# Performance work log

Hardware: AMD Instinct MI355X
Metric: run time of the kernel (lower is better)

Reference implementation:

```python
import jax, jax.numpy as jnp
import numpy as np

DIM = 768
HEADS = 8
HIDDEN = 3072
B, Hs, Ws = 16, 32, 32
N = Hs * Ws
LN_EPS = 1e-5


def setup_inputs() -> dict:
    key = jax.random.key(0)
    ks = jax.random.split(key, 10)
    s = lambda *sh: 0.02
    return {
        "x": jax.random.normal(ks[0], (B, N, DIM), jnp.float32),
        "Wq": jax.random.normal(ks[1], (DIM, DIM), jnp.float32) * 0.02,
        "temperature": jnp.ones((HEADS, 1, 1), jnp.float32),
        "fc1_w": jax.random.normal(ks[2], (HIDDEN, DIM), jnp.float32) * 0.02,
        "fc1_b": jnp.zeros((HIDDEN,), jnp.float32),
        "dw_w": jax.random.normal(ks[3], (HIDDEN, 1, 3, 3), jnp.float32) * 0.1,
        "dw_b": jnp.zeros((HIDDEN,), jnp.float32),
        "gamma": jnp.ones((HIDDEN,), jnp.float32),
        "fc2_w": jax.random.normal(ks[4], (DIM, HIDDEN), jnp.float32) * 0.02,
        "fc2_b": jnp.zeros((DIM,), jnp.float32),
        "ln_w": jnp.ones((DIM,), jnp.float32),
        "ln_b": jnp.zeros((DIM,), jnp.float32),
        "H": Hs,
        "W": Ws,
    }


def _dwconv(x, w, b, H, W):
    # x: (B, N, hidden) -> depthwise 3x3, pad 1 -> (B, N, hidden)
    Bn, Nn, Ch = x.shape
    img = x.transpose(0, 2, 1).reshape(Bn, Ch, H, W)
    out = jax.lax.conv_general_dilated(
        img, w, window_strides=(1, 1), padding=((1, 1), (1, 1)),
        dimension_numbers=("NCHW", "OIHW", "NCHW"), feature_group_count=Ch)
    out = out + b[None, :, None, None]
    return out.reshape(Bn, Ch, Nn).transpose(0, 2, 1)


def _layernorm(x, w, b):
    mu = x.mean(-1, keepdims=True)
    var = ((x - mu) ** 2).mean(-1, keepdims=True)
    return (x - mu) * jax.lax.rsqrt(var + LN_EPS) * w + b


def reference(x, Wq, temperature, fc1_w, fc1_b, dw_w, dw_b, gamma,
              fc2_w, fc2_b, ln_w, ln_b, H, W):
    # gpd_ratio == active_ratio == 1 -> pre/post scalings cancel
    Bn, Nn, C = x.shape
    h = temperature.shape[0]
    Ch = C // h
    # q/k/v heads: (B, h, N, Ch)
    q = (x @ Wq.T).reshape(Bn, Nn, h, Ch).transpose(0, 2, 1, 3)
    kv = x.reshape(Bn, Nn, h, Ch).transpose(0, 2, 1, 3)
    # channel attention: softmax over N, pool k over Ch, sigmoid gate
    qs = jax.nn.softmax(q, axis=-2).transpose(0, 1, 3, 2)      # (B,h,Ch,N)
    kp = jax.nn.softmax(kv, axis=-2).mean(-1, keepdims=True)    # (B,h,N,1)
    attn = jax.nn.sigmoid(qs @ kp) * temperature                # (B,h,Ch,1)
    # MLP on v (== x after scaling cancels): fc1 -> dwconv residual -> fc2 -> LN
    h1 = x @ fc1_w.T + fc1_b                                    # (B,N,hidden)
    h2 = gamma * _dwconv(h1, dw_w, dw_b, H, W) + h1
    v = _layernorm(h2 @ fc2_w.T + fc2_b, ln_w, ln_b)            # (B,N,C)
    v = v.reshape(Bn, Nn, h, Ch).transpose(0, 2, 1, 3)          # (B,h,N,Ch)
    prod = attn * v.transpose(0, 1, 3, 2)                       # (B,h,Ch,N)
    out = prod.transpose(0, 3, 1, 2).reshape(Bn, Nn, C)
    return out, prod.transpose(0, 1, 3, 2)
```

## Files before the change

### kernel.cpp

```cpp
#include <hip/hip_runtime.h>

#define BATCH 16
#define SEQ   1024
#define DIM   768
#define NHEAD 8
#define CHD   96
#define HID   3072
#define MTOT  (BATCH * SEQ)

using u16 = unsigned short;
typedef __attribute__((ext_vector_type(8))) short bf16x8;
typedef __attribute__((ext_vector_type(4))) float f32x4;

#define AS1 __attribute__((address_space(1)))
#define AS3 __attribute__((address_space(3)))

__device__ inline float bf2f(u16 u) {
    union { unsigned int i; float f; } v; v.i = ((unsigned int)u) << 16; return v.f;
}
__device__ inline u16 f2bf(float f) {
    union { float f; unsigned int i; } v; v.f = f;
    unsigned int r = v.i + 0x7FFFu + ((v.i >> 16) & 1u);
    return (u16)(r >> 16);
}

__device__ inline void gld16(const void* g, void* l) {
    __builtin_amdgcn_global_load_lds((AS1 const void*)g, (AS3 void*)l, 16, 0, 0);
}

__device__ inline void storeC(float* p, float v) { *p = v; }
__device__ inline void storeC(u16* p, float v) { *p = f2bf(v); }

template <bool HAS_BIAS, typename TC>
__global__ __launch_bounds__(256) void gemm_mfma(const u16* __restrict__ A,
                                                 const u16* __restrict__ B,
                                                 const float* __restrict__ bias,
                                                 TC* __restrict__ C,
                                                 int M, int N, int K) {
    __shared__ u16 As[128 * 32];
    __shared__ u16 Bs[128 * 32];
    const int tid = threadIdx.x;
    const int lane = tid & 63;
    const int m0 = blockIdx.y << 7, n0 = blockIdx.x << 7;
    const int wave = tid >> 6;
    const int wm = (wave >> 1) << 6, wn = (wave & 1) << 6;

    f32x4 acc[4][4] = {};

    const int row0 = tid >> 2;
    const int kc8 = (tid & 3) << 3;
    const u16* pa0 = A + (size_t)(m0 + row0) * K + kc8;
    const u16* pa1 = A + (size_t)(m0 + 64 + row0) * K + kc8;
    const u16* pb0 = B + (size_t)(n0 + row0) * K + kc8;
    const u16* pb1 = B + (size_t)(n0 + 64 + row0) * K + kc8;
    u16* da0 = &As[tid * 8];
    u16* da1 = &As[(256 + tid) * 8];
    u16* db0 = &Bs[tid * 8];
    u16* db1 = &Bs[(256 + tid) * 8];

    const int lrow = lane & 15;
    const int kgrp = (lane >> 4) << 3;

    for (int k0 = 0; k0 < K; k0 += 32) {
        gld16(pa0 + k0, da0);
        gld16(pa1 + k0, da1);
        gld16(pb0 + k0, db0);
        gld16(pb1 + k0, db1);
        __syncthreads();

        bf16x8 af[4], bfr[4];
#pragma unroll
        for (int i = 0; i < 4; ++i)
            af[i] = *(const bf16x8*)&As[(wm + i * 16 + lrow) * 32 + kgrp];
#pragma unroll
        for (int j = 0; j < 4; ++j)
            bfr[j] = *(const bf16x8*)&Bs[(wn + j * 16 + lrow) * 32 + kgrp];
#pragma unroll
        for (int i = 0; i < 4; ++i)
#pragma unroll
            for (int j = 0; j < 4; ++j)
                acc[i][j] = __builtin_amdgcn_mfma_f32_16x16x32_bf16(af[i], bfr[j], acc[i][j], 0, 0, 0);
        __syncthreads();
    }

    const int crow = (lane >> 4) << 2;
    const int ccol = lane & 15;
#pragma unroll
    for (int i = 0; i < 4; ++i) {
        const int gm = m0 + wm + i * 16 + crow;
#pragma unroll
        for (int j = 0; j < 4; ++j) {
            const int gn = n0 + wn + j * 16 + ccol;
            const float bv = HAS_BIAS ? bias[gn] : 0.f;
#pragma unroll
            for (int r = 0; r < 4; ++r)
                storeC(C + (size_t)(gm + r) * N + gn, acc[i][j][r] + bv);
        }
    }
}

__global__ __launch_bounds__(256) void cvt_f2bf(const float* __restrict__ in,
                                                u16* __restrict__ out, int n4) {
    int i = blockIdx.x * 256 + threadIdx.x;
    if (i >= n4) return;
    float4 v = reinterpret_cast<const float4*>(in)[i];
    ushort4 o;
    o.x = f2bf(v.x); o.y = f2bf(v.y); o.z = f2bf(v.z); o.w = f2bf(v.w);
    reinterpret_cast<ushort4*>(out)[i] = o;
}

template <typename T>
__global__ __launch_bounds__(256) void colsm_stats(const T* __restrict__ X,
                                                   float* __restrict__ Mo,
                                                   float* __restrict__ So,
                                                   int ncols) {
    const int tid = threadIdx.x, lane = tid & 63, chunk = tid >> 6;
    const int b = blockIdx.y;
    const int j = blockIdx.x * 64 + lane;
    const T* p = X + (size_t)b * SEQ * ncols + j;
    float m = -3.0e38f, s = 0.f;
    const int nEnd = (chunk + 1) << 8;
    for (int n = chunk << 8; n < nEnd; ++n) {
        float raw;
        if constexpr (sizeof(T) == 2) raw = bf2f(p[(size_t)n * ncols]);
        else raw = p[(size_t)n * ncols];
        float nm = fmaxf(m, raw);
        s = s * __expf(m - nm) + __expf(raw - nm);
        m = nm;
    }
    __shared__ float ms[4][64], ss[4][64];
    ms[chunk][lane] = m; ss[chunk][lane] = s;
    __syncthreads();
    if (tid < 64) {
        float M = fmaxf(fmaxf(ms[0][lane], ms[1][lane]), fmaxf(ms[2][lane], ms[3][lane]));
        float S = ss[0][lane] * __expf(ms[0][lane] - M) + ss[1][lane] * __expf(ms[1][lane] - M) +
                  ss[2][lane] * __expf(ms[2][lane] - M) + ss[3][lane] * __expf(ms[3][lane] - M);
        Mo[b * ncols + j] = M;
        So[b * ncols + j] = S;
    }
}

__global__ __launch_bounds__(256) void kp_k(const float* __restrict__ x,
                                            const float* __restrict__ Mx,
                                            const float* __restrict__ Sx,
                                            float* __restrict__ kp) {
    const int n = blockIdx.x, b = blockIdx.y, tid = threadIdx.x;
    __shared__ float p[DIM];
    const float* row = x + ((size_t)b * SEQ + n) * DIM;
#pragma unroll
    for (int q = 0; q < 3; ++q) {
        int j = tid + (q << 8);
        p[j] = __expf(row[j] - Mx[b * DIM + j]) / Sx[b * DIM + j];
    }
    __syncthreads();
    if (tid < NHEAD) {
        float s = 0.f;
        for (int c = 0; c < CHD; ++c) s += p[tid * CHD + c];
        kp[((size_t)b * NHEAD + tid) * SEQ + n] = s * (1.f / (float)CHD);
    }
}

__global__ __launch_bounds__(256) void attn_k(const u16* __restrict__ Q,
                                              const float* __restrict__ Mq,
                                              const float* __restrict__ Sq,
                                              const float* __restrict__ kp,
                                              const float* __restrict__ temp,
                                              float* __restrict__ attnv) {
    const int tid = threadIdx.x, lane = tid & 63, chunk = tid >> 6;
    const int b = blockIdx.y;
    const int j = blockIdx.x * 64 + lane;
    const int h = j / CHD;
    const float mq = Mq[b * DIM + j];
    const u16* qp = Q + (size_t)b * SEQ * DIM + j;
    const float* kpp = kp + ((size_t)b * NHEAD + h) * SEQ;
    float acc = 0.f;
    const int nEnd = (chunk + 1) << 8;
    for (int n = chunk << 8; n < nEnd; ++n)
        acc += __expf(bf2f(qp[(size_t)n * DIM]) - mq) * kpp[n];
    __shared__ float accs[4][64];
    accs[chunk][lane] = acc;
    __syncthreads();
    if (tid < 64) {
        float a = accs[0][lane] + accs[1][lane] + accs[2][lane] + accs[3][lane];
        float z = a / Sq[b * DIM + j];
        attnv[b * DIM + j] = temp[h] / (1.f + __expf(-z));
    }
}

__global__ __launch_bounds__(128) void dwconv_v(const u16* __restrict__ h1,
                                                const float* __restrict__ w,
                                                const float* __restrict__ dwb,
                                                const float* __restrict__ gamma,
                                                u16* __restrict__ h2) {
    const int g = blockIdx.x * 128 + threadIdx.x;
    const int y = blockIdx.y >> 2;
    const int xw0 = (blockIdx.y & 3) << 3;
    const int b = blockIdx.z;
    const int ch0 = g << 3;

    float wreg[8][9], bias2[8];
#pragma unroll
    for (int c = 0; c < 8; ++c) {
        const float gm = gamma[ch0 + c];
#pragma unroll
        for (int k = 0; k < 9; ++k) wreg[c][k] = gm * w[(ch0 + c) * 9 + k];
        wreg[c][4] += 1.0f;
        bias2[c] = gm * dwb[ch0 + c];
    }

    float acc[8][8];
#pragma unroll
    for (int xo = 0; xo < 8; ++xo)
#pragma unroll
        for (int c = 0; c < 8; ++c) acc[xo][c] = bias2[c];

    const u16* base = h1 + (size_t)b * SEQ * HID + ch0;
#pragma unroll
    for (int dy = 0; dy < 3; ++dy) {
        const int yy = y + dy - 1;
        if ((unsigned)yy > 31u) continue;
#pragma unroll
        for (int cr = -1; cr <= 8; ++cr) {
            const int col = xw0 + cr;
            if ((unsigned)col > 31u) continue;
            const uint4 v = *reinterpret_cast<const uint4*>(
                base + (size_t)((yy << 5) + col) * HID);
            float f[8];
            f[0] = bf2f((u16)(v.x & 0xffff)); f[1] = bf2f((u16)(v.x >> 16));
            f[2] = bf2f((u16)(v.y & 0xffff)); f[3] = bf2f((u16)(v.y >> 16));
            f[4] = bf2f((u16)(v.z & 0xffff)); f[5] = bf2f((u16)(v.w & 0xffff) * 0 + (u16)(v.z >> 16));
            f[6] = bf2f((u16)(v.w & 0xffff)); f[7] = bf2f((u16)(v.w >> 16));
            const int xlo = cr > 0 ? cr - 1 : 0;
            const int xhi = cr < 7 ? cr + 1 : 7;
#pragma unroll
            for (int xo = 0; xo < 8; ++xo) {
                if (xo < xlo || xo > xhi) continue;
                const int dx = cr - xo + 1;
#pragma unroll
                for (int c = 0; c < 8; ++c)
                    acc[xo][c] += f[c] * wreg[c][dy * 3 + dx];
            }
        }
    }

#pragma unroll
    for (int xo = 0; xo < 8; ++xo) {
        const int n = (y << 5) + xw0 + xo;
        uint4 o;
        o.x = (unsigned)f2bf(acc[xo][0]) | ((unsigned)f2bf(acc[xo][1]) << 16);
        o.y = (unsigned)f2bf(acc[xo][2]) | ((unsigned)f2bf(acc[xo][3]) << 16);
        o.z = (unsigned)f2bf(acc[xo][4]) | ((unsigned)f2bf(acc[xo][5]) << 16);
        o.w = (unsigned)f2bf(acc[xo][6]) | ((unsigned)f2bf(acc[xo][7]) << 16);
        *reinterpret_cast<uint4*>(h2 + ((size_t)b * SEQ + n) * HID + ch0) = o;
    }
}

__global__ __launch_bounds__(256) void ln_out_k(const u16* __restrict__ vpre,
                                                const float* __restrict__ lnw,
                                                const float* __restrict__ lnb,
                                                const float* __restrict__ attnv,
                                                float* __restrict__ out,
                                                float* __restrict__ out2) {
    const int n = blockIdx.x, b = blockIdx.y, tid = threadIdx.x;
    __shared__ float red[4];
    const u16* row = vpre + ((size_t)b * SEQ + n) * DIM;
    float v[3];
    float s = 0.f;
#pragma unroll
    for (int q = 0; q < 3; ++q) { v[q] = bf2f(row[tid + (q << 8)]); s += v[q]; }
#pragma unroll
    for (int o = 32; o; o >>= 1) s += __shfl_down(s, o, 64);
    if ((tid & 63) == 0) red[tid >> 6] = s;
    __syncthreads();
    const float mu = (red[0] + red[1] + red[2] + red[3]) * (1.f / (float)DIM);
    __syncthreads();
    float vs = 0.f;
#pragma unroll
    for (int q = 0; q < 3; ++q) { float d = v[q] - mu; vs += d * d; }
#pragma unroll
    for (int o = 32; o; o >>= 1) vs += __shfl_down(vs, o, 64);
    if ((tid & 63) == 0) red[tid >> 6] = vs;
    __syncthreads();
    const float rstd = rsqrtf((red[0] + red[1] + red[2] + red[3]) * (1.f / (float)DIM) + 1e-5f);
    const float* at = attnv + b * DIM;
    float* orow = out + ((size_t)b * SEQ + n) * DIM;
#pragma unroll
    for (int q = 0; q < 3; ++q) {
        int j = tid + (q << 8);
        float o = (v[q] - mu) * rstd * lnw[j] + lnb[j];
        o *= at[j];
        orow[j] = o;
        int h = j / CHD, c = j - h * CHD;
        out2[(((size_t)b * NHEAD + h) * SEQ + n) * CHD + c] = o;
    }
}

extern "C" void kernel_launch(void* const* d_in, const int* in_sizes, int n_in,
                              void* d_out, int out_size, void* d_ws, size_t ws_size,
                              hipStream_t stream) {
    const float* x     = (const float*)d_in[0];
    const float* Wq    = (const float*)d_in[1];
    const float* temp  = (const float*)d_in[2];
    const float* fc1w  = (const float*)d_in[3];
    const float* fc1b  = (const float*)d_in[4];
    const float* dww   = (const float*)d_in[5];
    const float* dwb   = (const float*)d_in[6];
    const float* gamma = (const float*)d_in[7];
    const float* fc2w  = (const float*)d_in[8];
    const float* fc2b  = (const float*)d_in[9];
    const float* lnw   = (const float*)d_in[10];
    const float* lnb   = (const float*)d_in[11];

    float* out  = (float*)d_out;
    float* out2 = out + (size_t)BATCH * SEQ * DIM;

    char* ws = (char*)d_ws;
    u16* xb     = (u16*)ws;
    u16* h1     = (u16*)(ws + 25165824);
    u16* Wqb    = (u16*)(ws + 125829120);
    u16* fc1wb  = (u16*)(ws + 127008768);
    u16* fc2wb  = (u16*)(ws + 131727360);
    float* Mx   = (float*)(ws + 136445952);
    float* Sx   = Mx + BATCH * DIM;
    float* Mq   = Sx + BATCH * DIM;
    float* Sq   = Mq + BATCH * DIM;
    float* kp   = Sq + BATCH * DIM;
    float* attnv = kp + BATCH * NHEAD * SEQ;
    u16* vpreb  = xb;

    u16* Qb = (u16*)d_out;
    u16* h2 = (u16*)d_out;

    cvt_f2bf<<<(MTOT * DIM / 4 + 255) / 256, 256, 0, stream>>>(x, xb, MTOT * DIM / 4);
    cvt_f2bf<<<(DIM * DIM / 4 + 255) / 256, 256, 0, stream>>>(Wq, Wqb, DIM * DIM / 4);
    cvt_f2bf<<<(HID * DIM / 4 + 255) / 256, 256, 0, stream>>>(fc1w, fc1wb, HID * DIM / 4);
    cvt_f2bf<<<(DIM * HID / 4 + 255) / 256, 256, 0, stream>>>(fc2w, fc2wb, DIM * HID / 4);

    gemm_mfma<false, u16><<<dim3(DIM / 128, MTOT / 128), 256, 0, stream>>>(
        xb, Wqb, nullptr, Qb, MTOT, DIM, DIM);
    colsm_stats<float><<<dim3(DIM / 64, BATCH), 256, 0, stream>>>(x, Mx, Sx, DIM);
    colsm_stats<u16><<<dim3(DIM / 64, BATCH), 256, 0, stream>>>(Qb, Mq, Sq, DIM);
    kp_k<<<dim3(SEQ, BATCH), 256, 0, stream>>>(x, Mx, Sx, kp);
    attn_k<<<dim3(DIM / 64, BATCH), 256, 0, stream>>>(Qb, Mq, Sq, kp, temp, attnv);

    gemm_mfma<true, u16><<<dim3(HID / 128, MTOT / 128), 256, 0, stream>>>(
        xb, fc1wb, fc1b, h1, MTOT, HID, DIM);
    dwconv_v<<<dim3(3, 128, BATCH), 128, 0, stream>>>(h1, dww, dwb, gamma, h2);
    gemm_mfma<true, u16><<<dim3(DIM / 128, MTOT / 128), 256, 0, stream>>>(
        h2, fc2wb, fc2b, vpreb, MTOT, DIM, HID);
    ln_out_k<<<dim3(SEQ, BATCH), 256, 0, stream>>>(vpreb, lnw, lnb, attnv, out, out2);
}
```

Baseline: 464.4 us.

## Rework GEMM with K=64 swizzled LDS tiles and XCD remap, fuse small kernels

```diff
diff --git a/kernel.cpp b/kernel.cpp
--- a/kernel.cpp
+++ b/kernel.cpp
@@ -28,63 +28,71 @@
     __builtin_amdgcn_global_load_lds((AS1 const void*)g, (AS3 void*)l, 16, 0, 0);
 }
 
-__device__ inline void storeC(float* p, float v) { *p = v; }
-__device__ inline void storeC(u16* p, float v) { *p = f2bf(v); }
-
-template <bool HAS_BIAS, typename TC>
-__global__ __launch_bounds__(256) void gemm_mfma(const u16* __restrict__ A,
-                                                 const u16* __restrict__ B,
-                                                 const float* __restrict__ bias,
-                                                 TC* __restrict__ C,
-                                                 int M, int N, int K) {
-    __shared__ u16 As[128 * 32];
-    __shared__ u16 Bs[128 * 32];
+template <bool HAS_BIAS>
+__global__ __launch_bounds__(256) void gemm128(const u16* __restrict__ A,
+                                               const u16* __restrict__ B,
+                                               const float* __restrict__ bias,
+                                               u16* __restrict__ C,
+                                               int M, int N, int K) {
+    __shared__ u16 As[128 * 64];
+    __shared__ u16 Bs[128 * 64];
     const int tid = threadIdx.x;
     const int lane = tid & 63;
-    const int m0 = blockIdx.y << 7, n0 = blockIdx.x << 7;
     const int wave = tid >> 6;
     const int wm = (wave >> 1) << 6, wn = (wave & 1) << 6;
 
+    const int nwg = gridDim.x;
+    const int wg = blockIdx.x;
+    const int lid = (wg & 7) * (nwg >> 3) + (wg >> 3);
+    const int nbx = N >> 7;
+    const int mb = lid / nbx, nb = lid - mb * nbx;
+    const int m0 = mb << 7, n0 = nb << 7;
+
+    const int srow = tid >> 3;
+    const int sce = ((tid & 7) << 3) ^ ((srow & 7) << 3);
+    const u16* pa = A + (size_t)(m0 + srow) * K + sce;
+    const u16* pb = B + (size_t)(n0 + srow) * K + sce;
+    const size_t rstep = (size_t)32 * K;
+
+    const int lrow = lane & 15;
+    const int ksl8 = (lane >> 4) << 3;
+    const int swz = (lrow & 7) << 3;
+    const int c0 = ksl8 ^ swz;
+    const int c1 = (32 + ksl8) ^ swz;
+
     f32x4 acc[4][4] = {};
 
-    const int row0 = tid >> 2;
-    const int kc8 = (tid & 3) << 3;
-    const u16* pa0 = A + (size_t)(m0 + row0) * K + kc8;
-    const u16* pa1 = A + (size_t)(m0 + 64 + row0) * K + kc8;
-    const u16* pb0 = B + (size_t)(n0 + row0) * K + kc8;
-    const u16* pb1 = B + (size_t)(n0 + 64 + row0) * K + kc8;
-    u16* da0 = &As[tid * 8];
-    u16* da1 = &As[(256 + tid) * 8];
-    u16* db0 = &Bs[tid * 8];
-    u16* db1 = &Bs[(256 + tid) * 8];
-
-    const int lrow = lane & 15;
-    const int kgrp = (lane >> 4) << 3;
-
-    for (int k0 = 0; k0 < K; k0 += 32) {
-        gld16(pa0 + k0, da0);
-        gld16(pa1 + k0, da1);
-        gld16(pb0 + k0, db0);
-        gld16(pb1 + k0, db1);
+    for (int k0 = 0; k0 < K; k0 += 64) {
+#pragma unroll
+        for (int q = 0; q < 4; ++q) {
+            gld16(pa + k0 + q * rstep, &As[q * 2048 + tid * 8]);
+            gld16(pb + k0 + q * rstep, &Bs[q * 2048 + tid * 8]);
+        }
         __syncthreads();
 
-        bf16x8 af[4], bfr[4];
+        bf16x8 af[4], bf[4];
+#pragma unroll
+        for (int i = 0; i < 4; ++i) af[i] = *(const bf16x8*)&As[(wm + i * 16 + lrow) * 64 + c0];
+#pragma unroll
+        for (int j = 0; j < 4; ++j) bf[j] = *(const bf16x8*)&Bs[(wn + j * 16 + lrow) * 64 + c0];
 #pragma unroll
         for (int i = 0; i < 4; ++i)
-            af[i] = *(const bf16x8*)&As[(wm + i * 16 + lrow) * 32 + kgrp];
-#pragma unroll
-        for (int j = 0; j < 4; ++j)
-            bfr[j] = *(const bf16x8*)&Bs[(wn + j * 16 + lrow) * 32 + kgrp];
+#pragma unroll
+            for (int j = 0; j < 4; ++j)
+                acc[i][j] = __builtin_amdgcn_mfma_f32_16x16x32_bf16(af[i], bf[j], acc[i][j], 0, 0, 0);
+#pragma unroll
+        for (int i = 0; i < 4; ++i) af[i] = *(const bf16x8*)&As[(wm + i * 16 + lrow) * 64 + c1];
+#pragma unroll
+        for (int j = 0; j < 4; ++j) bf[j] = *(const bf16x8*)&Bs[(wn + j * 16 + lrow) * 64 + c1];
 #pragma unroll
         for (int i = 0; i < 4; ++i)
 #pragma unroll
             for (int j = 0; j < 4; ++j)
-                acc[i][j] = __builtin_amdgcn_mfma_f32_16x16x32_bf16(af[i], bfr[j], acc[i][j], 0, 0, 0);
+                acc[i][j] = __builtin_amdgcn_mfma_f32_16x16x32_bf16(af[i], bf[j], acc[i][j], 0, 0, 0);
         __syncthreads();
     }
 
-    const int crow = (lane >> 4) << 2;
-    const int ccol = lane & 15;
+    const int crow = (lane >> 4) << 2, ccol = lane & 15;
 #pragma unroll
     for (int i = 0; i < 4; ++i) {
         const int gm = m0 + wm + i * 16 + crow;
@@ -94,36 +102,47 @@
             const float bv = HAS_BIAS ? bias[gn] : 0.f;
 #pragma unroll
             for (int r = 0; r < 4; ++r)
-                storeC(C + (size_t)(gm + r) * N + gn, acc[i][j][r] + bv);
+                C[(size_t)(gm + r) * N + gn] = f2bf(acc[i][j][r] + bv);
         }
     }
 }
 
-__global__ __launch_bounds__(256) void cvt_f2bf(const float* __restrict__ in,
-                                                u16* __restrict__ out, int n4) {
+__global__ __launch_bounds__(256) void cvt_all(const float* __restrict__ x,
+                                               const float* __restrict__ Wq,
+                                               const float* __restrict__ w1,
+                                               const float* __restrict__ w2,
+                                               u16* __restrict__ xb,
+                                               u16* __restrict__ Wqb,
+                                               u16* __restrict__ w1b,
+                                               u16* __restrict__ w2b) {
+    const int E0 = MTOT * DIM / 4;
+    const int E1 = E0 + DIM * DIM / 4;
+    const int E2 = E1 + HID * DIM / 4;
+    const int E3 = E2 + DIM * HID / 4;
     int i = blockIdx.x * 256 + threadIdx.x;
-    if (i >= n4) return;
-    float4 v = reinterpret_cast<const float4*>(in)[i];
+    if (i >= E3) return;
+    const float* in; u16* out; int k;
+    if (i < E0)      { in = x;  out = xb;  k = i; }
+    else if (i < E1) { in = Wq; out = Wqb; k = i - E0; }
+    else if (i < E2) { in = w1; out = w1b; k = i - E1; }
+    else             { in = w2; out = w2b; k = i - E2; }
+    float4 v = reinterpret_cast<const float4*>(in)[k];
     ushort4 o;
     o.x = f2bf(v.x); o.y = f2bf(v.y); o.z = f2bf(v.z); o.w = f2bf(v.w);
-    reinterpret_cast<ushort4*>(out)[i] = o;
-}
-
-template <typename T>
-__global__ __launch_bounds__(256) void colsm_stats(const T* __restrict__ X,
+    reinterpret_cast<ushort4*>(out)[k] = o;
+}
+
+__global__ __launch_bounds__(256) void colsm_stats(const u16* __restrict__ X,
                                                    float* __restrict__ Mo,
-                                                   float* __restrict__ So,
-                                                   int ncols) {
+                                                   float* __restrict__ So) {
     const int tid = threadIdx.x, lane = tid & 63, chunk = tid >> 6;
     const int b = blockIdx.y;
     const int j = blockIdx.x * 64 + lane;
-    const T* p = X + (size_t)b * SEQ * ncols + j;
+    const u16* p = X + (size_t)b * SEQ * DIM + j;
     float m = -3.0e38f, s = 0.f;
     const int nEnd = (chunk + 1) << 8;
     for (int n = chunk << 8; n < nEnd; ++n) {
-        float raw;
-        if constexpr (sizeof(T) == 2) raw = bf2f(p[(size_t)n * ncols]);
-        else raw = p[(size_t)n * ncols];
+        float raw = bf2f(p[(size_t)n * DIM]);
         float nm = fmaxf(m, raw);
         s = s * __expf(m - nm) + __expf(raw - nm);
         m = nm;
@@ -135,22 +154,22 @@
         float M = fmaxf(fmaxf(ms[0][lane], ms[1][lane]), fmaxf(ms[2][lane], ms[3][lane]));
         float S = ss[0][lane] * __expf(ms[0][lane] - M) + ss[1][lane] * __expf(ms[1][lane] - M) +
                   ss[2][lane] * __expf(ms[2][lane] - M) + ss[3][lane] * __expf(ms[3][lane] - M);
-        Mo[b * ncols + j] = M;
-        So[b * ncols + j] = S;
-    }
-}
-
-__global__ __launch_bounds__(256) void kp_k(const float* __restrict__ x,
+        Mo[b * DIM + j] = M;
+        So[b * DIM + j] = S;
+    }
+}
+
+__global__ __launch_bounds__(256) void kp_k(const u16* __restrict__ x,
                                             const float* __restrict__ Mx,
                                             const float* __restrict__ Sx,
                                             float* __restrict__ kp) {
     const int n = blockIdx.x, b = blockIdx.y, tid = threadIdx.x;
     __shared__ float p[DIM];
-    const float* row = x + ((size_t)b * SEQ + n) * DIM;
+    const u16* row = x + ((size_t)b * SEQ + n) * DIM;
 #pragma unroll
     for (int q = 0; q < 3; ++q) {
         int j = tid + (q << 8);
-        p[j] = __expf(row[j] - Mx[b * DIM + j]) / Sx[b * DIM + j];
+        p[j] = __expf(bf2f(row[j]) - Mx[b * DIM + j]) / Sx[b * DIM + j];
     }
     __syncthreads();
     if (tid < NHEAD) {
@@ -160,29 +179,39 @@
     }
 }
 
-__global__ __launch_bounds__(256) void attn_k(const u16* __restrict__ Q,
-                                              const float* __restrict__ Mq,
-                                              const float* __restrict__ Sq,
-                                              const float* __restrict__ kp,
-                                              const float* __restrict__ temp,
-                                              float* __restrict__ attnv) {
+__global__ __launch_bounds__(256) void qattn_k(const u16* __restrict__ Q,
+                                               const float* __restrict__ kp,
+                                               const float* __restrict__ temp,
+                                               float* __restrict__ attnv) {
     const int tid = threadIdx.x, lane = tid & 63, chunk = tid >> 6;
     const int b = blockIdx.y;
     const int j = blockIdx.x * 64 + lane;
     const int h = j / CHD;
-    const float mq = Mq[b * DIM + j];
     const u16* qp = Q + (size_t)b * SEQ * DIM + j;
     const float* kpp = kp + ((size_t)b * NHEAD + h) * SEQ;
-    float acc = 0.f;
+    float m = -3.0e38f, s = 0.f, a = 0.f;
     const int nEnd = (chunk + 1) << 8;
-    for (int n = chunk << 8; n < nEnd; ++n)
-        acc += __expf(bf2f(qp[(size_t)n * DIM]) - mq) * kpp[n];
-    __shared__ float accs[4][64];
-    accs[chunk][lane] = acc;
+    for (int n = chunk << 8; n < nEnd; ++n) {
+        float q = bf2f(qp[(size_t)n * DIM]);
+        float nm = fmaxf(m, q);
+        float sc = __expf(m - nm), e = __expf(q - nm);
+        s = s * sc + e;
+        a = a * sc + e * kpp[n];
+        m = nm;
+    }
+    __shared__ float ms[4][64], ss[4][64], as_[4][64];
+    ms[chunk][lane] = m; ss[chunk][lane] = s; as_[chunk][lane] = a;
     __syncthreads();
     if (tid < 64) {
-        float a = accs[0][lane] + accs[1][lane] + accs[2][lane] + accs[3][lane];
-        float z = a / Sq[b * DIM + j];
+        float M = fmaxf(fmaxf(ms[0][lane], ms[1][lane]), fmaxf(ms[2][lane], ms[3][lane]));
+        float S = 0.f, A = 0.f;
+#pragma unroll
+        for (int c = 0; c < 4; ++c) {
+            float sc = __expf(ms[c][lane] - M);
+            S += ss[c][lane] * sc;
+            A += as_[c][lane] * sc;
+        }
+        float z = A / S;
         attnv[b * DIM + j] = temp[h] / (1.f + __expf(-z));
     }
 }
@@ -228,7 +257,7 @@
             float f[8];
             f[0] = bf2f((u16)(v.x & 0xffff)); f[1] = bf2f((u16)(v.x >> 16));
             f[2] = bf2f((u16)(v.y & 0xffff)); f[3] = bf2f((u16)(v.y >> 16));
-            f[4] = bf2f((u16)(v.z & 0xffff)); f[5] = bf2f((u16)(v.w & 0xffff) * 0 + (u16)(v.z >> 16));
+            f[4] = bf2f((u16)(v.z & 0xffff)); f[5] = bf2f((u16)(v.z >> 16));
             f[6] = bf2f((u16)(v.w & 0xffff)); f[7] = bf2f((u16)(v.w >> 16));
             const int xlo = cr > 0 ? cr - 1 : 0;
             const int xhi = cr < 7 ? cr + 1 : 7;
@@ -322,31 +351,29 @@
     u16* fc2wb  = (u16*)(ws + 131727360);
     float* Mx   = (float*)(ws + 136445952);
     float* Sx   = Mx + BATCH * DIM;
-    float* Mq   = Sx + BATCH * DIM;
-    float* Sq   = Mq + BATCH * DIM;
-    float* kp   = Sq + BATCH * DIM;
+    float* kp   = Sx + BATCH * DIM;
     float* attnv = kp + BATCH * NHEAD * SEQ;
     u16* vpreb  = xb;
 
     u16* Qb = (u16*)d_out;
     u16* h2 = (u16*)d_out;
 
-    cvt_f2bf<<<(MTOT * DIM / 4 + 255) / 256, 256, 0, stream>>>(x, xb, MTOT * DIM / 4);
-    cvt_f2bf<<<(DIM * DIM / 4 + 255) / 256, 256, 0, stream>>>(Wq, Wqb, DIM * DIM / 4);
-    cvt_f2bf<<<(HID * DIM / 4 + 255) / 256, 256, 0, stream>>>(fc1w, fc1wb, HID * DIM / 4);
-    cvt_f2bf<<<(DIM * HID / 4 + 255) / 256, 256, 0, stream>>>(fc2w, fc2wb, DIM * HID / 4);
-
-    gemm_mfma<false, u16><<<dim3(DIM / 128, MTOT / 128), 256, 0, stream>>>(
+    {
+        const int tot4 = (MTOT * DIM + DIM * DIM + HID * DIM + DIM * HID) / 4;
+        cvt_all<<<(tot4 + 255) / 256, 256, 0, stream>>>(
+            x, Wq, fc1w, fc2w, xb, Wqb, fc1wb, fc2wb);
+    }
+
+    gemm128<false><<<(MTOT / 128) * (DIM / 128), 256, 0, stream>>>(
         xb, Wqb, nullptr, Qb, MTOT, DIM, DIM);
-    colsm_stats<float><<<dim3(DIM / 64, BATCH), 256, 0, stream>>>(x, Mx, Sx, DIM);
-    colsm_stats<u16><<<dim3(DIM / 64, BATCH), 256, 0, stream>>>(Qb, Mq, Sq, DIM);
-    kp_k<<<dim3(SEQ, BATCH), 256, 0, stream>>>(x, Mx, Sx, kp);
-    attn_k<<<dim3(DIM / 64, BATCH), 256, 0, stream>>>(Qb, Mq, Sq, kp, temp, attnv);
-
-    gemm_mfma<true, u16><<<dim3(HID / 128, MTOT / 128), 256, 0, stream>>>(
+    colsm_stats<<<dim3(DIM / 64, BATCH), 256, 0, stream>>>(xb, Mx, Sx);
+    kp_k<<<dim3(SEQ, BATCH), 256, 0, stream>>>(xb, Mx, Sx, kp);
+    qattn_k<<<dim3(DIM / 64, BATCH), 256, 0, stream>>>(Qb, kp, temp, attnv);
+
+    gemm128<true><<<(MTOT / 128) * (HID / 128), 256, 0, stream>>>(
         xb, fc1wb, fc1b, h1, MTOT, HID, DIM);
     dwconv_v<<<dim3(3, 128, BATCH), 128, 0, stream>>>(h1, dww, dwb, gamma, h2);
-    gemm_mfma<true, u16><<<dim3(DIM / 128, MTOT / 128), 256, 0, stream>>>(
+    gemm128<true><<<(MTOT / 128) * (DIM / 128), 256, 0, stream>>>(
         h2, fc2wb, fc2b, vpreb, MTOT, DIM, HID);
     ln_out_k<<<dim3(SEQ, BATCH), 256, 0, stream>>>(vpreb, lnw, lnb, attnv, out, out2);
 }
```

After: 425.9 us. -8.3%, faster.
